# Performance work log

Measured on AMD Instinct MI355X. Metric: run time of the kernel, lower is better.

## Reference

```python
import jax, jax.numpy as jnp
import numpy as np

N_HEADS = 8


def _update_state(demand, dyn, idx, cap0):
    # subtract demand of chosen node; reset to full capacity when returning to depot (node 0)
    cur = jnp.take_along_axis(demand, idx[:, None], axis=1)  # (B,1)
    dyn = dyn - cur
    dyn = jnp.where((idx == 0)[:, None], cap0, dyn)
    return jax.lax.stop_gradient(dyn)  # mirrors .detach() in the torch repo


def _update_mask(demand, dyn, idx, mask1):
    B, N = demand.shape
    go_depot = (idx == 0)
    mask1 = mask1.at[jnp.arange(B), idx].set(1.0)          # mark visited
    depot_mask = go_depot.astype(mask1.dtype)              # cannot stay at depot
    done = mask1[:, 1:].sum(axis=1) >= (N - 1)             # all customers served
    depot_mask = jnp.where(done, jnp.zeros_like(depot_mask), depot_mask)
    mask1 = mask1.at[:, 0].set(depot_mask)
    mask = jnp.minimum(mask1 + (demand > dyn).astype(mask1.dtype), 1.0)
    mask = mask.at[:, 0].set(depot_mask)                   # depot never capacity-masked
    return mask, mask1


def _pointer_logits(state_t, context, mask, T, wq, wk, wv, wo, wkp):
    # multi-head glimpse + single-head tanh-clipped pointer (Kool/Lei-style)
    B, N, D = context.shape
    H = wq.shape[1]
    hd = H // N_HEADS
    q = (state_t @ wq).reshape(B, N_HEADS, hd)
    k = (context @ wk).reshape(B, N, N_HEADS, hd)
    v = (context @ wv).reshape(B, N, N_HEADS, hd)
    u = jnp.einsum('bhd,bnhd->bhn', q, k) * (hd ** -0.5)   # (B,H,N)
    u = jnp.where(mask[:, None, :] > 0, -jnp.inf, u)
    a = jax.nn.softmax(u, axis=-1)
    glimpse = jnp.einsum('bhn,bnhd->bhd', a, v).reshape(B, H) @ wo  # (B,H)
    kp = context @ wkp                                     # (B,N,H)
    comp = jnp.einsum('bd,bnd->bn', glimpse, kp) * (H ** -0.5)
    logits = 10.0 * jnp.tanh(comp) / T
    return jnp.where(mask > 0, -jnp.inf, logits)           # (B,N)


def _decode(encoder_inputs, pool, capacity, demand, fc_w, fc1_w, wq, wk, wv, wo, wkp, T, n_steps, num_samples, greedy):
    B, N, D = encoder_inputs.shape
    cap0 = capacity[0, 0]
    base_key = jax.random.key(1234)
    actions_all, logps_all = [], []
    for s in range(num_samples):
        mask1 = jnp.zeros((B, N), encoder_inputs.dtype)
        dyn = jnp.broadcast_to(capacity, (B, 1)).astype(encoder_inputs.dtype)
        idx0 = jnp.zeros((B,), jnp.int32)
        mask, mask1 = _update_mask(demand, dyn, idx0, mask1)   # i == 0 pre-mask
        inp = encoder_inputs[:, 0, :]

        def step(carry, key):
            inp, dyn, mask, mask1, pool = carry
            dec = jnp.concatenate([inp, dyn], axis=-1) @ fc_w  # fc
            pool = pool @ fc1_w  # NB: fc1 re-applied to pool EVERY step (faithful quirk of source)
            dec = dec + pool
            logits = _pointer_logits(dec, encoder_inputs, mask, T, wq, wk, wv, wo, wkp)
            if greedy:
                idx = jnp.argmax(logits, axis=-1).astype(jnp.int32)
            else:
                idx = jax.random.categorical(key, logits).astype(jnp.int32)
            log_p = jnp.take_along_axis(jax.nn.log_softmax(logits, axis=-1), idx[:, None], axis=1)[:, 0]
            dyn = _update_state(demand, dyn, idx, cap0)
            mask, mask1 = _update_mask(demand, dyn, idx, mask1)
            # faithful to source: compares against full seq_len, so is_done is always 0
            is_done = (mask1[:, 1:].sum(axis=1) >= N).astype(log_p.dtype)
            log_p = log_p * (1.0 - is_done)
            inp = jnp.take_along_axis(encoder_inputs, idx[:, None, None], axis=1)[:, 0, :]
            return (inp, dyn, mask, mask1, pool), (idx, log_p)

        keys = jax.random.split(jax.random.fold_in(base_key, s), n_steps)
        (inp, dyn, mask, mask1, pool), (acts, lps) = jax.lax.scan(
            step, (inp, dyn, mask, mask1, pool), keys)
        actions_all.append(acts.T)          # (B, n_steps)
        logps_all.append(lps.sum(axis=0))   # (B,)
    return jnp.stack(actions_all), jnp.stack(logps_all)


def setup_inputs() -> dict:
    key = jax.random.key(0)
    ks = jax.random.split(key, 10)
    B, N, D = 256, 51, 128
    H = D
    s = 0.08  # ~ xavier std for 128x128
    enc = jax.random.normal(ks[0], (B, N, D), jnp.float32)
    pool = jax.random.normal(ks[1], (B, H), jnp.float32)
    capacity = jnp.ones((1, 1), jnp.float32)
    demand = jax.random.uniform(ks[2], (B, N), jnp.float32) * 0.3
    demand = demand.at[:, 0].set(0.0)  # depot has no demand
    return dict(
        encoder_inputs=enc, pool=pool, capacity=capacity, demand=demand,
        fc_w=jax.random.normal(ks[3], (H + 1, H), jnp.float32) * s,
        fc1_w=jax.random.normal(ks[4], (H, H), jnp.float32) * s,
        wq=jax.random.normal(ks[5], (H, H), jnp.float32) * s,
        wk=jax.random.normal(ks[6], (D, H), jnp.float32) * s,
        wv=jax.random.normal(ks[7], (D, H), jnp.float32) * s,
        wo=jax.random.normal(ks[8], (H, H), jnp.float32) * s,
        wkp=jax.random.normal(ks[9], (D, H), jnp.float32) * s,
        T=jnp.asarray(1.0, jnp.float32), n_steps=60, num_samples=1, greedy=0)


def reference(encoder_inputs, pool, capacity, demand, fc_w, fc1_w, wq, wk, wv, wo, wkp, T, n_steps, num_samples, greedy):
    return _decode(encoder_inputs, pool, capacity, demand, fc_w, fc1_w, wq, wk, wv, wo, wkp,
                   T, n_steps, num_samples, greedy)
```

## Files before the change

kernel.cpp:

```cpp
#include <hip/hip_runtime.h>

#define NN 51
#define DD 128
#define RS 132
#define NT 64
#define NINFF (-__builtin_inff())

__device__ __forceinline__ float dot4(const float4 a, const float4 b) {
  return a.x * b.x + a.y * b.y + a.z * b.z + a.w * b.w;
}

template<int CTRL>
__device__ __forceinline__ float dppf(float x, float idf) {
  return __int_as_float(__builtin_amdgcn_update_dpp(
      __float_as_int(idf), __float_as_int(x), CTRL, 0xf, 0xf, false));
}
__device__ __forceinline__ float readlanef(float x, int lane) {
  return __int_as_float(__builtin_amdgcn_readlane(__float_as_int(x), lane));
}
__device__ __forceinline__ float bcast63(float x) { return readlanef(x, 63); }
__device__ __forceinline__ float wave_max_b(float x) {
  x = fmaxf(x, dppf<0x111>(x, NINFF));
  x = fmaxf(x, dppf<0x112>(x, NINFF));
  x = fmaxf(x, dppf<0x114>(x, NINFF));
  x = fmaxf(x, dppf<0x118>(x, NINFF));
  x = fmaxf(x, dppf<0x142>(x, NINFF));
  x = fmaxf(x, dppf<0x143>(x, NINFF));
  return bcast63(x);
}
__device__ __forceinline__ float wave_sum_b(float x) {
  x += dppf<0x111>(x, 0.f);
  x += dppf<0x112>(x, 0.f);
  x += dppf<0x114>(x, 0.f);
  x += dppf<0x118>(x, 0.f);
  x += dppf<0x142>(x, 0.f);
  x += dppf<0x143>(x, 0.f);
  return bcast63(x);
}
__device__ __forceinline__ float row16_sum(float x) {
  x += dppf<0x111>(x, 0.f);
  x += dppf<0x112>(x, 0.f);
  x += dppf<0x114>(x, 0.f);
  x += dppf<0x118>(x, 0.f);
  return x;
}
__device__ __forceinline__ float quad_sum(float x) {
  x += dppf<0xB1>(x, 0.f);
  x += dppf<0x4E>(x, 0.f);
  return x;
}

__device__ __forceinline__ void tf2x32(unsigned k0, unsigned k1, unsigned &x0, unsigned &x1) {
  const unsigned ks2 = k0 ^ k1 ^ 0x1BD11BDAu;
  const unsigned ka[5] = {k1, ks2, k0, k1, ks2};
  const unsigned kb[5] = {ks2 + 1u, k0 + 2u, k1 + 3u, ks2 + 4u, k0 + 5u};
  x0 += k0; x1 += k1;
#pragma unroll
  for (int g = 0; g < 5; ++g) {
    const int r0 = (g & 1) ? 17 : 13;
    const int r1 = (g & 1) ? 29 : 15;
    const int r2 = (g & 1) ? 16 : 26;
    const int r3 = (g & 1) ? 24 : 6;
    x0 += x1; x1 = (x1 << r0) | (x1 >> (32 - r0)); x1 ^= x0;
    x0 += x1; x1 = (x1 << r1) | (x1 >> (32 - r1)); x1 ^= x0;
    x0 += x1; x1 = (x1 << r2) | (x1 >> (32 - r2)); x1 ^= x0;
    x0 += x1; x1 = (x1 << r3) | (x1 >> (32 - r3)); x1 ^= x0;
    x0 += ka[g]; x1 += kb[g];
  }
}

__device__ __forceinline__ float gumbel_from(unsigned k0, unsigned k1, unsigned ctr) {
  unsigned x0 = 0u, x1 = ctr;
  tf2x32(k0, k1, x0, x1);
  const unsigned bits = x0 ^ x1;
  const float fl = __uint_as_float((bits >> 9) | 0x3f800000u) - 1.0f;
  const float TINY = 1.17549435e-38f;
  const float uu = fmaxf(TINY, fl + TINY);
  return -logf(-logf(uu));
}

__global__ __launch_bounds__(512, 1) void decode_kernel(
    const float* __restrict__ enc, const float* __restrict__ pool_in,
    const float* __restrict__ cap_p, const float* __restrict__ demand,
    const float* __restrict__ fc_w, const float* __restrict__ fc1,
    const float* __restrict__ wq, const float* __restrict__ wk,
    const float* __restrict__ wv, const float* __restrict__ wo,
    const float* __restrict__ wkp, const float* __restrict__ T_p,
    const int* __restrict__ ns_p, const int* __restrict__ greedy_p,
    float* __restrict__ out) {
  __shared__ __align__(16) float Ksh[NN * RS];
  __shared__ __align__(16) float Vsh[64 * RS];
  __shared__ __align__(16) float KP2sh[NN * RS];
  __shared__ __align__(16) float EQsh[NN * RS];
  __shared__ __align__(16) float qpoolL[NT * DD];
  __shared__ __align__(16) float uL[8 * 64];
  __shared__ __align__(16) float pcb2[2][8 * 64];
  __shared__ __align__(16) float poolB[2][DD];
  __shared__ __align__(16) float wrowL[DD];
  __shared__ __align__(16) float partF[512];
  __shared__ float demL[NN];
  __shared__ float pgumL[2][NN];
  __shared__ unsigned keysL[2 * NT];

  const int b = blockIdx.x, tid = threadIdx.x;
  const int Bn = gridDim.x;
  const int w = tid >> 6, l = tid & 63;
  int ns = *ns_p; if (ns > NT) ns = NT;
  const int greedy = *greedy_p;
  const float Tval = *T_p;
  const float cap0 = *cap_p;

  {
    const float4* src = (const float4*)(enc + (size_t)b * NN * DD);
    float4* dst = (float4*)qpoolL;
    for (int e = tid; e < NN * DD / 4; e += 512) dst[e] = src[e];
  }
  if (tid < 128) poolB[0][tid] = pool_in[b * DD + tid];
  for (int e = tid; e < 13 * RS; e += 512) Vsh[51 * RS + e] = 0.f;
  if (tid < NN)  demL[tid] = demand[b * NN + tid];
  if (tid < ns) {
    unsigned a0 = 0u, a1 = 0u;
    tf2x32(0u, 1234u, a0, a1);
    unsigned x0 = 0u, x1 = (unsigned)tid;
    tf2x32(a0, a1, x0, x1);
    keysL[2 * tid] = x0; keysL[2 * tid + 1] = x1;
  }
  __syncthreads();

  float dem_l = (l < NN) ? demL[l] : 0.f;

  if (!greedy && tid >= 448) {
    const int gl = tid - 448;
    if (gl < NN)
      pgumL[0][gl] = gumbel_from(keysL[0], keysL[1], (unsigned)(b * NN + gl));
  }
  {
    const int c = tid & 127, qd = tid >> 7;
    const float* fr = fc_w + 128 * DD;
    float s = 0.f;
    for (int j = qd * 32; j < qd * 32 + 32; ++j) s += fr[j] * wq[j * DD + c];
    partF[tid] = s;
  }
  __syncthreads();
  if (tid < 128)
    wrowL[tid] = partF[tid] + partF[tid + 128] + partF[tid + 256] + partF[tid + 384];

  const int g4 = tid >> 7, cc = tid & 127;
  const int n0 = g4 * 13, cnt13 = (g4 == 3) ? 12 : 13;

  {
    float aK[13], aV[13], aT1[13], aT2[13];
#pragma unroll
    for (int r = 0; r < 13; ++r) { aK[r] = 0.f; aV[r] = 0.f; aT1[r] = 0.f; aT2[r] = 0.f; }
    for (int i = 0; i < DD; i += 4) {
      const float k0 = wk[(i + 0) * DD + cc], k1 = wk[(i + 1) * DD + cc];
      const float k2 = wk[(i + 2) * DD + cc], k3 = wk[(i + 3) * DD + cc];
      const float v0 = wv[(i + 0) * DD + cc], v1 = wv[(i + 1) * DD + cc];
      const float v2 = wv[(i + 2) * DD + cc], v3 = wv[(i + 3) * DD + cc];
      const float f0 = fc_w[(i + 0) * DD + cc], f1 = fc_w[(i + 1) * DD + cc];
      const float f2 = fc_w[(i + 2) * DD + cc], f3 = fc_w[(i + 3) * DD + cc];
      const float p0 = wkp[(i + 0) * DD + cc], p1 = wkp[(i + 1) * DD + cc];
      const float p2 = wkp[(i + 2) * DD + cc], p3 = wkp[(i + 3) * DD + cc];
#pragma unroll
      for (int r = 0; r < 13; ++r) {
        if (r < cnt13) {
          const float4 e4 = *(const float4*)&qpoolL[(n0 + r) * DD + i];
          aK[r]  += e4.x * k0 + e4.y * k1 + e4.z * k2 + e4.w * k3;
          aV[r]  += e4.x * v0 + e4.y * v1 + e4.z * v2 + e4.w * v3;
          aT1[r] += e4.x * f0 + e4.y * f1 + e4.z * f2 + e4.w * f3;
          aT2[r] += e4.x * p0 + e4.y * p1 + e4.z * p2 + e4.w * p3;
        }
      }
    }
#pragma unroll
    for (int r = 0; r < 13; ++r) {
      if (r < cnt13) {
        Ksh[(n0 + r) * RS + cc]   = aK[r];
        Vsh[(n0 + r) * RS + cc]   = aV[r];
        EQsh[(n0 + r) * RS + cc]  = aT1[r];
        KP2sh[(n0 + r) * RS + cc] = aT2[r];
      }
    }
  }
  __syncthreads();

  {
    float aEQ[13], aKP[13];
#pragma unroll
    for (int r = 0; r < 13; ++r) { aEQ[r] = 0.f; aKP[r] = 0.f; }
    for (int i = 0; i < DD; i += 4) {
      const float q0 = wq[(i + 0) * DD + cc], q1 = wq[(i + 1) * DD + cc];
      const float q2 = wq[(i + 2) * DD + cc], q3 = wq[(i + 3) * DD + cc];
      const float4 w4 = *(const float4*)&wo[cc * DD + i];
#pragma unroll
      for (int r = 0; r < 13; ++r) {
        if (r < cnt13) {
          const float4 t1 = *(const float4*)&EQsh[(n0 + r) * RS + i];
          const float4 t2 = *(const float4*)&KP2sh[(n0 + r) * RS + i];
          aEQ[r] += t1.x * q0 + t1.y * q1 + t1.z * q2 + t1.w * q3;
          aKP[r] += dot4(t2, w4);
        }
      }
    }
    __syncthreads();
#pragma unroll
    for (int r = 0; r < 13; ++r) {
      if (r < cnt13) {
        EQsh[(n0 + r) * RS + cc]  = aEQ[r];
        KP2sh[(n0 + r) * RS + cc] = aKP[r];
      }
    }
  }
  __syncthreads();

  const int rowc = (l < NN) ? l : 0;
  const float4* kbase = (const float4*)&Ksh[rowc * RS + w * 16];
  const float4 Kr0 = kbase[0], Kr1 = kbase[1], Kr2 = kbase[2], Kr3 = kbase[3];
  const float4* pbase = (const float4*)&KP2sh[rowc * RS + w * 16];
  const float4 Pr0 = pbase[0], Pr1 = pbase[1], Pr2 = pbase[2], Pr3 = pbase[3];
  const int dq = l >> 4, nn0 = l & 15;
  const float4 Vr0 = *(const float4*)&Vsh[(nn0 +  0) * RS + w * 16 + dq * 4];
  const float4 Vr1 = *(const float4*)&Vsh[(nn0 + 16) * RS + w * 16 + dq * 4];
  const float4 Vr2 = *(const float4*)&Vsh[(nn0 + 32) * RS + w * 16 + dq * 4];
  const float4 Vr3 = *(const float4*)&Vsh[(nn0 + 48) * RS + w * 16 + dq * 4];
  const float4* wbase = (const float4*)&wrowL[w * 16];
  const float4 Wr0 = wbase[0], Wr1 = wbase[1], Wr2 = wbase[2], Wr3 = wbase[3];

  {
    const int colC = tid >> 2, qrt = tid & 3;
    float wfr[32];
#pragma unroll
    for (int i = 0; i < 32; ++i) wfr[i] = fc1[(qrt * 32 + i) * DD + colC];
    int cur = 0;
    for (int t = 0; t < ns; ++t) {
      float s = 0.f;
#pragma unroll
      for (int i = 0; i < 32; ++i) s += poolB[cur][qrt * 32 + i] * wfr[i];
      s = quad_sum(s);
      if (qrt == 0) {
        qpoolL[t * DD + colC] = s;
        poolB[cur ^ 1][colC] = s;
      }
      cur ^= 1;
      __syncthreads();
    }
    const int qch = (ns + 3) >> 2;
    const int r0 = g4 * qch;
    const int rcnt = (ns - r0 < qch) ? (ns - r0) : qch;
    float acc[16];
#pragma unroll
    for (int r = 0; r < 16; ++r) acc[r] = 0.f;
    for (int i = 0; i < DD; i += 4) {
      const float q0 = wq[(i + 0) * DD + cc], q1 = wq[(i + 1) * DD + cc];
      const float q2 = wq[(i + 2) * DD + cc], q3 = wq[(i + 3) * DD + cc];
#pragma unroll
      for (int r = 0; r < 16; ++r) {
        if (r < rcnt) {
          const float4 p4 = *(const float4*)&qpoolL[(r0 + r) * DD + i];
          acc[r] += p4.x * q0 + p4.y * q1 + p4.z * q2 + p4.w * q3;
        }
      }
    }
    __syncthreads();
#pragma unroll
    for (int r = 0; r < 16; ++r)
      if (r < rcnt) qpoolL[(r0 + r) * DD + cc] = acc[r];
  }
  __syncthreads();

  int m1 = (l == 0) ? 1 : 0;
  float dynr = cap0, depotr = 1.f, lpacc0 = 0.f, lpacc1 = 0.f;
  float4 qv0, qv1, qv2, qv3;
  {
    const float4* eq = (const float4*)&EQsh[0 * RS + w * 16];
    const float4* qp = (const float4*)&qpoolL[0 * DD + w * 16];
    qv0.x = eq[0].x + cap0 * Wr0.x + qp[0].x; qv0.y = eq[0].y + cap0 * Wr0.y + qp[0].y;
    qv0.z = eq[0].z + cap0 * Wr0.z + qp[0].z; qv0.w = eq[0].w + cap0 * Wr0.w + qp[0].w;
    qv1.x = eq[1].x + cap0 * Wr1.x + qp[1].x; qv1.y = eq[1].y + cap0 * Wr1.y + qp[1].y;
    qv1.z = eq[1].z + cap0 * Wr1.z + qp[1].z; qv1.w = eq[1].w + cap0 * Wr1.w + qp[1].w;
    qv2.x = eq[2].x + cap0 * Wr2.x + qp[2].x; qv2.y = eq[2].y + cap0 * Wr2.y + qp[2].y;
    qv2.z = eq[2].z + cap0 * Wr2.z + qp[2].z; qv2.w = eq[2].w + cap0 * Wr2.w + qp[2].w;
    qv3.x = eq[3].x + cap0 * Wr3.x + qp[3].x; qv3.y = eq[3].y + cap0 * Wr3.y + qp[3].y;
    qv3.z = eq[3].z + cap0 * Wr3.z + qp[3].z; qv3.w = eq[3].w + cap0 * Wr3.w + qp[3].w;
  }

  for (int t = 0; t < ns; ++t) {
    {
      const bool maskedl =
          (l == 0) ? (depotr > 0.f)
          : (l < NN ? ((m1 != 0) || (dem_l > dynr)) : true);
      float u1 = NINFF;
      if (l < NN && !maskedl)
        u1 = 0.25f * ((dot4(Kr0, qv0) + dot4(Kr1, qv1)) +
                      (dot4(Kr2, qv2) + dot4(Kr3, qv3)));
      const float mx = wave_max_b(u1);
      const float e = (u1 > NINFF) ? expf(u1 - mx) : 0.f;
      const float S = wave_sum_b(e);
      uL[w * 64 + l] = e;
      asm volatile("s_waitcnt lgkmcnt(0)" ::: "memory");
      __builtin_amdgcn_sched_barrier(0);
      const float a0 = uL[w * 64 + nn0];
      const float a1 = uL[w * 64 + nn0 + 16];
      const float a2 = uL[w * 64 + nn0 + 32];
      const float a3 = uL[w * 64 + nn0 + 48];
      float ax = a0 * Vr0.x + a1 * Vr1.x + a2 * Vr2.x + a3 * Vr3.x;
      float ay = a0 * Vr0.y + a1 * Vr1.y + a2 * Vr2.y + a3 * Vr3.y;
      float az = a0 * Vr0.z + a1 * Vr1.z + a2 * Vr2.z + a3 * Vr3.z;
      float aw = a0 * Vr0.w + a1 * Vr1.w + a2 * Vr2.w + a3 * Vr3.w;
      ax = row16_sum(ax) / S; ay = row16_sum(ay) / S;
      az = row16_sum(az) / S; aw = row16_sum(aw) / S;
      const float g0  = readlanef(ax, 15), g1  = readlanef(ay, 15);
      const float g2  = readlanef(az, 15), g3  = readlanef(aw, 15);
      const float g4g = readlanef(ax, 31), g5  = readlanef(ay, 31);
      const float g6  = readlanef(az, 31), g7  = readlanef(aw, 31);
      const float g8  = readlanef(ax, 47), g9  = readlanef(ay, 47);
      const float g10 = readlanef(az, 47), g11 = readlanef(aw, 47);
      const float g12 = readlanef(ax, 63), g13 = readlanef(ay, 63);
      const float g14 = readlanef(az, 63), g15 = readlanef(aw, 63);
      const float part =
          ((Pr0.x * g0  + Pr0.y * g1  + Pr0.z * g2  + Pr0.w * g3) +
           (Pr1.x * g4g + Pr1.y * g5  + Pr1.z * g6  + Pr1.w * g7)) +
          ((Pr2.x * g8  + Pr2.y * g9  + Pr2.z * g10 + Pr2.w * g11) +
           (Pr3.x * g12 + Pr3.y * g13 + Pr3.z * g14 + Pr3.w * g15));
      pcb2[t & 1][w * 64 + l] = part;
    }
    __syncthreads();
    {
      if (w == 7 && !greedy && t + 1 < ns && l < NN)
        pgumL[(t + 1) & 1][l] =
            gumbel_from(keysL[2 * (t + 1)], keysL[2 * (t + 1) + 1],
                        (unsigned)(b * NN + l));
      const float* pcb = pcb2[t & 1];
      float lgv = NINFF;
      {
        const float p0 = pcb[0 * 64 + l], p1 = pcb[1 * 64 + l];
        const float p2 = pcb[2 * 64 + l], p3 = pcb[3 * 64 + l];
        const float p4 = pcb[4 * 64 + l], p5 = pcb[5 * 64 + l];
        const float p6 = pcb[6 * 64 + l], p7 = pcb[7 * 64 + l];
        const float comp = (((p0 + p1) + (p2 + p3)) + ((p4 + p5) + (p6 + p7))) *
                           0.08838834764831845f;
        const float lg = (10.f * tanhf(comp)) / Tval;
        const bool maskedn =
            (l == 0) ? (depotr > 0.f) : ((m1 != 0) || (dem_l > dynr));
        if (l < NN) lgv = maskedn ? NINFF : lg;
      }
      const float pg = (!greedy && l < NN) ? pgumL[t & 1][l] : 0.f;
      const float pv = (l < NN) ? (lgv + pg) : NINFF;
      const float vmax = wave_max_b(pv);
      const unsigned long long Meq = __ballot(pv == vmax);
      const int best = __ffsll(Meq) - 1;
      if (l == best) m1 = 1;
      const unsigned long long M = __ballot(m1 != 0);
      const int cntv = (int)__popcll(M & ~1ull);
      const float dem_b = readlanef(dem_l, best);
      dynr = (best == 0) ? cap0 : (dynr - dem_b);
      depotr = (best == 0) ? 1.f : 0.f;
      if (cntv >= NN - 1) depotr = 0.f;
      if (w == 0) {
        lpacc0 += readlanef(lgv, best);
        const float mm = wave_max_b(lgv);
        const float ee = wave_sum_b((lgv > NINFF) ? expf(lgv - mm) : 0.f);
        lpacc1 += mm + logf(ee);
        if (l == 0) out[b * ns + t] = (float)best;
      }
      const int qidx = (t + 1 < ns) ? (t + 1) : 0;
      const float4* eq = (const float4*)&EQsh[best * RS + w * 16];
      const float4* qp = (const float4*)&qpoolL[qidx * DD + w * 16];
      qv0.x = eq[0].x + dynr * Wr0.x + qp[0].x; qv0.y = eq[0].y + dynr * Wr0.y + qp[0].y;
      qv0.z = eq[0].z + dynr * Wr0.z + qp[0].z; qv0.w = eq[0].w + dynr * Wr0.w + qp[0].w;
      qv1.x = eq[1].x + dynr * Wr1.x + qp[1].x; qv1.y = eq[1].y + dynr * Wr1.y + qp[1].y;
      qv1.z = eq[1].z + dynr * Wr1.z + qp[1].z; qv1.w = eq[1].w + dynr * Wr1.w + qp[1].w;
      qv2.x = eq[2].x + dynr * Wr2.x + qp[2].x; qv2.y = eq[2].y + dynr * Wr2.y + qp[2].y;
      qv2.z = eq[2].z + dynr * Wr2.z + qp[2].z; qv2.w = eq[2].w + dynr * Wr2.w + qp[2].w;
      qv3.x = eq[3].x + dynr * Wr3.x + qp[3].x; qv3.y = eq[3].y + dynr * Wr3.y + qp[3].y;
      qv3.z = eq[3].z + dynr * Wr3.z + qp[3].z; qv3.w = eq[3].w + dynr * Wr3.w + qp[3].w;
    }
  }
  if (tid == 0) out[Bn * ns + b] = lpacc0 - lpacc1;
}

extern "C" void kernel_launch(void* const* d_in, const int* in_sizes, int n_in,
                              void* d_out, int out_size, void* d_ws, size_t ws_size,
                              hipStream_t stream) {
  const float* enc    = (const float*)d_in[0];
  const float* pool   = (const float*)d_in[1];
  const float* cap    = (const float*)d_in[2];
  const float* dem    = (const float*)d_in[3];
  const float* fc_w   = (const float*)d_in[4];
  const float* fc1_w  = (const float*)d_in[5];
  const float* wq     = (const float*)d_in[6];
  const float* wk     = (const float*)d_in[7];
  const float* wv     = (const float*)d_in[8];
  const float* wo     = (const float*)d_in[9];
  const float* wkp    = (const float*)d_in[10];
  const float* Tp     = (const float*)d_in[11];
  const int*   nsp    = (const int*)d_in[12];
  const int*   greedy = (const int*)d_in[14];
  float* out = (float*)d_out;

  const int B = in_sizes[1] / DD;

  hipLaunchKernelGGL(decode_kernel, dim3(B), dim3(512), 0, stream,
                     enc, pool, cap, dem, fc_w, fc1_w, wq, wk, wv, wo, wkp,
                     Tp, nsp, greedy, out);
}
```

Baseline: 206.1 us.

## Precompute Gumbel noise upfront, shuffle softmax weights, batch action stores

All per-step Gumbel noise values are now computed before the decode loop into a shared table, instead of one wave generating the next step's noise inside each step. The attention weights are exchanged with wave shuffles instead of a round trip through LDS with an explicit wait. The log-prob reduction moves to wave 1 so wave 0 carries less serial work. Action indices are buffered in LDS and written out once at the end. The next-step query-pool loads are hoisted earlier in the step. The upfront table costs extra LDS and startup time, and the V padding is reduced by clamping the row index.

```diff
diff --git a/kernel.cpp b/kernel.cpp
--- a/kernel.cpp
+++ b/kernel.cpp
@@ -89,17 +89,16 @@
     const int* __restrict__ ns_p, const int* __restrict__ greedy_p,
     float* __restrict__ out) {
   __shared__ __align__(16) float Ksh[NN * RS];
-  __shared__ __align__(16) float Vsh[64 * RS];
+  __shared__ __align__(16) float Vsh[52 * RS];
   __shared__ __align__(16) float KP2sh[NN * RS];
   __shared__ __align__(16) float EQsh[NN * RS];
   __shared__ __align__(16) float qpoolL[NT * DD];
-  __shared__ __align__(16) float uL[8 * 64];
   __shared__ __align__(16) float pcb2[2][8 * 64];
   __shared__ __align__(16) float poolB[2][DD];
   __shared__ __align__(16) float wrowL[DD];
-  __shared__ __align__(16) float partF[512];
+  __shared__ __align__(16) float gumT[NT * NN];
   __shared__ float demL[NN];
-  __shared__ float pgumL[2][NN];
+  __shared__ float actsL[NT];
   __shared__ unsigned keysL[2 * NT];
 
   const int b = blockIdx.x, tid = threadIdx.x;
@@ -109,6 +108,7 @@
   const int greedy = *greedy_p;
   const float Tval = *T_p;
   const float cap0 = *cap_p;
+  float* partF = &pcb2[0][0];
 
   {
     const float4* src = (const float4*)(enc + (size_t)b * NN * DD);
@@ -116,7 +116,7 @@
     for (int e = tid; e < NN * DD / 4; e += 512) dst[e] = src[e];
   }
   if (tid < 128) poolB[0][tid] = pool_in[b * DD + tid];
-  for (int e = tid; e < 13 * RS; e += 512) Vsh[51 * RS + e] = 0.f;
+  if (tid < RS)  Vsh[51 * RS + tid] = 0.f;
   if (tid < NN)  demL[tid] = demand[b * NN + tid];
   if (tid < ns) {
     unsigned a0 = 0u, a1 = 0u;
@@ -129,10 +129,11 @@
 
   float dem_l = (l < NN) ? demL[l] : 0.f;
 
-  if (!greedy && tid >= 448) {
-    const int gl = tid - 448;
-    if (gl < NN)
-      pgumL[0][gl] = gumbel_from(keysL[0], keysL[1], (unsigned)(b * NN + gl));
+  if (!greedy) {
+    for (int job = tid; job < ns * NN; job += 512) {
+      const int t = job / NN, n = job - t * NN;
+      gumT[job] = gumbel_from(keysL[2 * t], keysL[2 * t + 1], (unsigned)(b * NN + n));
+    }
   }
   {
     const int c = tid & 127, qd = tid >> 7;
@@ -218,11 +219,12 @@
   const float4 Kr0 = kbase[0], Kr1 = kbase[1], Kr2 = kbase[2], Kr3 = kbase[3];
   const float4* pbase = (const float4*)&KP2sh[rowc * RS + w * 16];
   const float4 Pr0 = pbase[0], Pr1 = pbase[1], Pr2 = pbase[2], Pr3 = pbase[3];
-  const int dq = l >> 4, nn0 = l & 15;
+  const int nn0 = l & 15, dq = l >> 4;
+  const int vr3 = (nn0 + 48 <= 51) ? (nn0 + 48) : 51;
   const float4 Vr0 = *(const float4*)&Vsh[(nn0 +  0) * RS + w * 16 + dq * 4];
   const float4 Vr1 = *(const float4*)&Vsh[(nn0 + 16) * RS + w * 16 + dq * 4];
   const float4 Vr2 = *(const float4*)&Vsh[(nn0 + 32) * RS + w * 16 + dq * 4];
-  const float4 Vr3 = *(const float4*)&Vsh[(nn0 + 48) * RS + w * 16 + dq * 4];
+  const float4 Vr3 = *(const float4*)&Vsh[vr3 * RS + w * 16 + dq * 4];
   const float4* wbase = (const float4*)&wrowL[w * 16];
   const float4 Wr0 = wbase[0], Wr1 = wbase[1], Wr2 = wbase[2], Wr3 = wbase[3];
 
@@ -295,14 +297,11 @@
                       (dot4(Kr2, qv2) + dot4(Kr3, qv3)));
       const float mx = wave_max_b(u1);
       const float e = (u1 > NINFF) ? expf(u1 - mx) : 0.f;
+      const float a0 = __shfl(e, nn0);
+      const float a1 = __shfl(e, nn0 + 16);
+      const float a2 = __shfl(e, nn0 + 32);
+      const float a3 = __shfl(e, nn0 + 48);
       const float S = wave_sum_b(e);
-      uL[w * 64 + l] = e;
-      asm volatile("s_waitcnt lgkmcnt(0)" ::: "memory");
-      __builtin_amdgcn_sched_barrier(0);
-      const float a0 = uL[w * 64 + nn0];
-      const float a1 = uL[w * 64 + nn0 + 16];
-      const float a2 = uL[w * 64 + nn0 + 32];
-      const float a3 = uL[w * 64 + nn0 + 48];
       float ax = a0 * Vr0.x + a1 * Vr1.x + a2 * Vr2.x + a3 * Vr3.x;
       float ay = a0 * Vr0.y + a1 * Vr1.y + a2 * Vr2.y + a3 * Vr3.y;
       float az = a0 * Vr0.z + a1 * Vr1.z + a2 * Vr2.z + a3 * Vr3.z;
@@ -326,10 +325,10 @@
     }
     __syncthreads();
     {
-      if (w == 7 && !greedy && t + 1 < ns && l < NN)
-        pgumL[(t + 1) & 1][l] =
-            gumbel_from(keysL[2 * (t + 1)], keysL[2 * (t + 1) + 1],
-                        (unsigned)(b * NN + l));
+      const int qidx = (t + 1 < ns) ? (t + 1) : 0;
+      const float4* qp = (const float4*)&qpoolL[qidx * DD + w * 16];
+      const float4 qp0 = qp[0], qp1 = qp[1], qp2 = qp[2], qp3 = qp[3];
+      const float pg = (!greedy && l < NN) ? gumT[t * NN + l] : 0.f;
       const float* pcb = pcb2[t & 1];
       float lgv = NINFF;
       {
@@ -344,7 +343,6 @@
             (l == 0) ? (depotr > 0.f) : ((m1 != 0) || (dem_l > dynr));
         if (l < NN) lgv = maskedn ? NINFF : lg;
       }
-      const float pg = (!greedy && l < NN) ? pgumL[t & 1][l] : 0.f;
       const float pv = (l < NN) ? (lgv + pg) : NINFF;
       const float vmax = wave_max_b(pv);
       const unsigned long long Meq = __ballot(pv == vmax);
@@ -356,27 +354,27 @@
       dynr = (best == 0) ? cap0 : (dynr - dem_b);
       depotr = (best == 0) ? 1.f : 0.f;
       if (cntv >= NN - 1) depotr = 0.f;
-      if (w == 0) {
+      if (w == 1) {
         lpacc0 += readlanef(lgv, best);
         const float mm = wave_max_b(lgv);
         const float ee = wave_sum_b((lgv > NINFF) ? expf(lgv - mm) : 0.f);
         lpacc1 += mm + logf(ee);
-        if (l == 0) out[b * ns + t] = (float)best;
-      }
-      const int qidx = (t + 1 < ns) ? (t + 1) : 0;
+      }
+      if (w == 0 && l == 0) actsL[t] = (float)best;
       const float4* eq = (const float4*)&EQsh[best * RS + w * 16];
-      const float4* qp = (const float4*)&qpoolL[qidx * DD + w * 16];
-      qv0.x = eq[0].x + dynr * Wr0.x + qp[0].x; qv0.y = eq[0].y + dynr * Wr0.y + qp[0].y;
-      qv0.z = eq[0].z + dynr * Wr0.z + qp[0].z; qv0.w = eq[0].w + dynr * Wr0.w + qp[0].w;
-      qv1.x = eq[1].x + dynr * Wr1.x + qp[1].x; qv1.y = eq[1].y + dynr * Wr1.y + qp[1].y;
-      qv1.z = eq[1].z + dynr * Wr1.z + qp[1].z; qv1.w = eq[1].w + dynr * Wr1.w + qp[1].w;
-      qv2.x = eq[2].x + dynr * Wr2.x + qp[2].x; qv2.y = eq[2].y + dynr * Wr2.y + qp[2].y;
-      qv2.z = eq[2].z + dynr * Wr2.z + qp[2].z; qv2.w = eq[2].w + dynr * Wr2.w + qp[2].w;
-      qv3.x = eq[3].x + dynr * Wr3.x + qp[3].x; qv3.y = eq[3].y + dynr * Wr3.y + qp[3].y;
-      qv3.z = eq[3].z + dynr * Wr3.z + qp[3].z; qv3.w = eq[3].w + dynr * Wr3.w + qp[3].w;
-    }
-  }
-  if (tid == 0) out[Bn * ns + b] = lpacc0 - lpacc1;
+      qv0.x = eq[0].x + dynr * Wr0.x + qp0.x; qv0.y = eq[0].y + dynr * Wr0.y + qp0.y;
+      qv0.z = eq[0].z + dynr * Wr0.z + qp0.z; qv0.w = eq[0].w + dynr * Wr0.w + qp0.w;
+      qv1.x = eq[1].x + dynr * Wr1.x + qp1.x; qv1.y = eq[1].y + dynr * Wr1.y + qp1.y;
+      qv1.z = eq[1].z + dynr * Wr1.z + qp1.z; qv1.w = eq[1].w + dynr * Wr1.w + qp1.w;
+      qv2.x = eq[2].x + dynr * Wr2.x + qp2.x; qv2.y = eq[2].y + dynr * Wr2.y + qp2.y;
+      qv2.z = eq[2].z + dynr * Wr2.z + qp2.z; qv2.w = eq[2].w + dynr * Wr2.w + qp2.w;
+      qv3.x = eq[3].x + dynr * Wr3.x + qp3.x; qv3.y = eq[3].y + dynr * Wr3.y + qp3.y;
+      qv3.z = eq[3].z + dynr * Wr3.z + qp3.z; qv3.w = eq[3].w + dynr * Wr3.w + qp3.w;
+    }
+  }
+  __syncthreads();
+  if (w == 0 && l < ns) out[b * ns + l] = actsL[l];
+  if (w == 1 && l == 0) out[Bn * ns + b] = lpacc0 - lpacc1;
 }
 
 extern "C" void kernel_launch(void* const* d_in, const int* in_sizes, int n_in,
```

Measured after the change: 197.9 us. 1.04x faster.
